# Kernel optimization log

Measured on AMD Instinct MI355X. Metric: run time of the kernel, lower is better.

The kernel has to match this reference:

```python
import jax, jax.numpy as jnp
import numpy as np

ANG = 5   # angular resolution (u = v = 5, n = 25 views)
CH = 64   # input channels
D = 2 * CH  # spa_dim + ang_dim + fre_dim = c/2 + c/2 + c = 128
NEG = -1e15


def _l2(x):
    # torch F.normalize over the contraction axis (last axis of folded layout)
    n = jnp.sqrt(jnp.sum(x * x, axis=-1, keepdims=True))
    return x / jnp.maximum(n, 1e-12)


def setup_inputs() -> dict:
    key = jax.random.key(0)
    ks = jax.random.split(key, 8)
    b, c, n, h, w = 4, CH, ANG * ANG, 32, 32
    d = D
    return {
        "x_lf": jax.random.normal(ks[0], (b, c, n, h, w), jnp.float32),
        "x_hf": jax.random.normal(ks[1], (b, c, n, h, w), jnp.float32),
        "W_in": jax.random.normal(ks[2], (c, d), jnp.float32) / np.sqrt(c).astype(np.float32),
        "W_kv": jax.random.normal(ks[3], (c, d), jnp.float32) / np.sqrt(c).astype(np.float32),
        "ln_g": jnp.ones((d,), jnp.float32),
        "ln_b": jnp.zeros((d,), jnp.float32),
        "W_m1": jax.random.normal(ks[4], (d, d), jnp.float32) / np.sqrt(d).astype(np.float32),
        "W_m2": jax.random.normal(ks[5], (d, d), jnp.float32) / np.sqrt(d).astype(np.float32),
        "W_out": jax.random.normal(ks[6], (d, c), jnp.float32) / np.sqrt(d).astype(np.float32),
    }


def _attend(fold, unfold, tq, tk, tv):
    # fold(t): (b, cc, u*v, h, w) -> (b, M, K); k/v use the same folding
    qf = _l2(fold(tq))            # q normalized over contraction axis
    kf = _l2(fold(tk))            # k normalized over contraction axis (dim=-2 of k^T)
    vf = fold(tv)
    att = jnp.einsum('bmk,bnk->bmn', qf, kf)   # (b, M, M)
    M = att.shape[-1]
    tril = jnp.tril(jnp.ones((M, M), bool))    # causal mask over folded axis
    att = jax.nn.softmax(jnp.where(tril, att, NEG), axis=-1)
    return unfold(att @ vf) + tv               # residual with token_v


def reference(x_lf, x_hf, W_in, W_kv, ln_g, ln_b, W_m1, W_m2, W_out):
    b, c, n, h, w = x_hf.shape
    u = v = ANG
    d = W_in.shape[1]

    def to_tokens(x, W):
        # 'b c (u v) h w -> (b u v) (h w) c' ; Linear ; back to 'b d (u v) h w'
        xt = x.reshape(b, c, u, v, h, w).transpose(0, 2, 3, 4, 5, 1).reshape(b * u * v, h * w, c)
        y = xt @ W
        return y.reshape(b, u, v, h, w, d).transpose(0, 5, 1, 2, 3, 4).reshape(b, d, u * v, h, w)

    q = to_tokens(x_hf, W_in)
    kv = to_tokens(x_lf, W_kv)
    cq = d // 4
    sf_q, af_q, sa_q = q[:, :cq], q[:, cq:2 * cq], q[:, 2 * cq:]
    sf_kv, af_kv, sa_kv = kv[:, :cq], kv[:, cq:2 * cq], kv[:, 2 * cq:]

    # SpatialFrequency: 'b c (u v) h w -> b (c h) (w u v)'
    def sf_fold(t):
        cc = t.shape[1]
        return t.reshape(b, cc, u, v, h, w).transpose(0, 1, 4, 5, 2, 3).reshape(b, cc * h, w * u * v)
    def sf_unfold(t):
        cc = t.shape[1] // h
        return t.reshape(b, cc, h, w, u, v).transpose(0, 1, 4, 5, 2, 3).reshape(b, cc, u * v, h, w)

    # AngularFrequency: 'b c (u v) h w -> b (c u) (h v w)'
    def af_fold(t):
        cc = t.shape[1]
        return t.reshape(b, cc, u, v, h, w).transpose(0, 1, 2, 4, 3, 5).reshape(b, cc * u, h * v * w)
    def af_unfold(t):
        cc = t.shape[1] // u
        return t.reshape(b, cc, u, h, v, w).transpose(0, 1, 2, 4, 3, 5).reshape(b, cc, u * v, h, w)

    # SpatialAngular: 'b c (u v) h w -> b (h u) (c v w)'
    def sa_fold(t):
        cc = t.shape[1]
        return t.reshape(b, cc, u, v, h, w).transpose(0, 4, 2, 1, 3, 5).reshape(b, h * u, cc * v * w)
    def sa_unfold(t):
        cc = t.shape[2] // (v * w) if t.ndim == 3 else t.shape[1]
        t = t.reshape(b, h, u, cc, v, w)
        return t.transpose(0, 3, 2, 4, 1, 5).reshape(b, cc, u * v, h, w)

    sf = _attend(sf_fold, sf_unfold, sf_q, sf_kv, sf_kv)
    af = _attend(af_fold, af_unfold, af_q, af_kv, af_kv)
    sa = _attend(sa_fold, sa_unfold, sa_q, sa_kv, sa_kv)

    cat = jnp.concatenate([sf, af, sa], axis=1)  # (b, d, n, h, w)
    ct = cat.reshape(b, d, u, v, h, w).transpose(0, 2, 3, 4, 5, 1).reshape(b * u * v, h * w, d)

    # c_mlp: LayerNorm -> Linear -> ReLU -> Linear (dropout is identity in eval)
    mu = jnp.mean(ct, axis=-1, keepdims=True)
    var = jnp.mean(jnp.square(ct - mu), axis=-1, keepdims=True)
    ln = (ct - mu) / jnp.sqrt(var + 1e-5) * ln_g + ln_b
    mlp = jax.nn.relu(ln @ W_m1) @ W_m2
    out_t = (mlp + ct) @ W_out  # residual then output projection

    out = out_t.reshape(b, u, v, h, w, -1).transpose(0, 5, 1, 2, 3, 4).reshape(b, -1, u * v, h, w)
    return out
```

## Files before the change

kernel.cpp:

```cpp
#include <hip/hip_runtime.h>

#define NSP   25600
#define HWC   1024

typedef __attribute__((ext_vector_type(8))) short bf8;
typedef __attribute__((ext_vector_type(4))) float f4;
#define MFMA(a,b,c) __builtin_amdgcn_mfma_f32_16x16x32_bf16(a, b, c, 0, 0, 0)
typedef unsigned short u16;

__device__ __forceinline__ u16 f2b(float f) {
    union { float f; unsigned u; } v; v.f = f;
    unsigned r = v.u + 0x7fffu + ((v.u >> 16) & 1u);
    return (u16)(r >> 16);
}
__device__ __forceinline__ float b2f(u16 h) {
    union { unsigned u; float f; } v; v.u = ((unsigned)h) << 16;
    return v.f;
}

__device__ __forceinline__ long row_base(int att, int b, int m) {
    if (att == 0) { int cc = m >> 5, h = m & 31;   return ((long)(b*128 + cc))*NSP + h*32; }
    else if (att == 1) { int cc = m / 5, u = m - cc*5; return ((long)(b*128 + 32 + cc))*NSP + u*5120; }
    else { int h = m / 5, u = m - h*5;            return ((long)(b*128 + 64))*NSP + u*5120 + h*32; }
}
__device__ __forceinline__ long chunk_off(int att, int kc) {
    if (att == 0) return (long)kc * 1024;
    else if (att == 1) return (long)kc * 32;
    else { int cc = kc / 5, v = kc - cc*5; return (long)cc*NSP + v*1024; }
}

__global__ __launch_bounds__(256) void k_prep(
        const float* __restrict__ Wi, const float* __restrict__ Wk,
        const float* __restrict__ W1, const float* __restrict__ W2,
        const float* __restrict__ Wo, u16* __restrict__ wbt) {
    int e = blockIdx.x * 256 + threadIdx.x;
    const float* src; int base, K, N;
    if (e < 8192)       { src = Wi; base = 0;     K = 64;  N = 128; }
    else if (e < 16384) { src = Wk; base = 8192;  K = 64;  N = 128; }
    else if (e < 32768) { src = W1; base = 16384; K = 128; N = 128; }
    else if (e < 49152) { src = W2; base = 32768; K = 128; N = 128; }
    else                { src = Wo; base = 49152; K = 128; N = 64;  }
    int local = e - base, n = local / K, k = local - n * K;
    wbt[e] = f2b(src[k * N + n]);
}

__global__ __launch_bounds__(256) void k_tokens(
        const float* __restrict__ x_hf, const float* __restrict__ x_lf,
        const u16* __restrict__ wbt,
        u16* __restrict__ qb, u16* __restrict__ kvb) {
    int s0 = blockIdx.x * 64, b = blockIdx.y, which = blockIdx.z;
    const float* x  = which ? x_lf : x_hf;
    const u16* Wb = wbt + (which ? 8192 : 0);
    u16* out = which ? kvb : qb;
    __shared__ u16 Axs[64 * 72];
    __shared__ u16 Wl [128 * 72];
    int tid = threadIdx.x;
    for (int g = tid; g < 1024; g += 256) {
        int d = g >> 3, c8 = (g & 7) * 8;
        *(bf8*)&Wl[d * 72 + c8] = *(const bf8*)(Wb + d * 64 + c8);
    }
    for (int g = tid; g < 1024; g += 256) {
        int s = g & 63, c4 = (g >> 6) * 4;
        long xb = ((long)(b * 64 + c4)) * NSP + s0 + s;
        ushort4 pk;
        pk.x = f2b(x[xb]);
        pk.y = f2b(x[xb + NSP]);
        pk.z = f2b(x[xb + 2 * NSP]);
        pk.w = f2b(x[xb + 3 * NSP]);
        *(ushort4*)&Axs[s * 72 + c4] = pk;
    }
    __syncthreads();
    int w = tid >> 6, l = tid & 63, quad = l >> 4, col = l & 15;
    f4 z = {0.f, 0.f, 0.f, 0.f};
    f4 acc[8]; for (int i = 0; i < 8; ++i) acc[i] = z;
#pragma unroll
    for (int kc = 0; kc < 2; ++kc) {
        bf8 a = *(bf8*)&Axs[(w * 16 + col) * 72 + kc * 32 + quad * 8];
#pragma unroll
        for (int nt = 0; nt < 8; ++nt) {
            bf8 bb = *(bf8*)&Wl[(nt * 16 + col) * 72 + kc * 32 + quad * 8];
            acc[nt] = MFMA(a, bb, acc[nt]);
        }
    }
#pragma unroll
    for (int nt = 0; nt < 8; ++nt) {
        int d = nt * 16 + col;
        long base = ((long)(b * 128 + d)) * NSP + s0 + w * 16 + quad * 4;
        ushort4 pk;
        pk.x = f2b(acc[nt][0]); pk.y = f2b(acc[nt][1]);
        pk.z = f2b(acc[nt][2]); pk.w = f2b(acc[nt][3]);
        *(ushort4*)(out + base) = pk;
    }
}

__global__ __launch_bounds__(256) void k_vt_norms(
        const u16* __restrict__ qb, const u16* __restrict__ kvb,
        u16* __restrict__ vt0, u16* __restrict__ vt1, u16* __restrict__ vt2,
        float* __restrict__ nq, float* __restrict__ nk) {
    int x = blockIdx.x, b = blockIdx.y;
    int tid = threadIdx.x;
    if (x < 3200) {
        int att, kc, pt, P, KC; u16* vt;
        if (x < 800)       { att = 0; kc = x >> 5; pt = (x & 31) * 32; P = 1024; KC = 25;  vt = vt0; }
        else if (x < 1600) { int x2 = x - 800;  att = 1; kc = x2 / 5; pt = (x2 - kc * 5) * 32; P = 160; KC = 160; vt = vt1; }
        else               { int x3 = x - 1600; att = 2; kc = x3 / 5; pt = (x3 - kc * 5) * 32; P = 160; KC = 320; vt = vt2; }
        long co = chunk_off(att, kc);
        __shared__ u16 T[32 * 36];
        {
            int r = tid >> 3, fq = (tid & 7) * 4;
            ushort4 e = *(const ushort4*)(kvb + row_base(att, b, pt + r) + co + fq);
            *(ushort4*)&T[r * 36 + fq] = e;
        }
        __syncthreads();
        {
            int f = tid >> 3, p4 = (tid & 7) * 4;
            ushort4 pk;
            pk.x = T[(p4    ) * 36 + f];
            pk.y = T[(p4 + 1) * 36 + f];
            pk.z = T[(p4 + 2) * 36 + f];
            pk.w = T[(p4 + 3) * 36 + f];
            *(ushort4*)(vt + ((long)b * KC + kc) * 32 * P + (long)f * P + pt + p4) = pk;
        }
    } else {
        int x2 = x - 3200;
        int which = x2 >= 336;
        int g = which ? x2 - 336 : x2;
        int att, m0, KC;
        if (g < 256)      { att = 0; m0 = g * 4;         KC = 25;  }
        else if (g < 296) { att = 1; m0 = (g - 256) * 4; KC = 160; }
        else              { att = 2; m0 = (g - 296) * 4; KC = 320; }
        const u16* src = which ? kvb : qb;
        float* dst = which ? nk : nq;
        int w = tid >> 6, lane = tid & 63;
        int m = m0 + w;
        long base = row_base(att, b, m);
        int K = KC * 32;
        float s = 0.f;
        for (int k8 = lane * 8; k8 < K; k8 += 512) {
            bf8 v = *(const bf8*)(src + base + chunk_off(att, k8 >> 5) + (k8 & 31));
#pragma unroll
            for (int j = 0; j < 8; ++j) { float f = b2f(((u16*)&v)[j]); s += f * f; }
        }
        for (int o = 32; o >= 1; o >>= 1) s += __shfl_xor(s, o);
        if (lane == 0) {
            int off = (att == 0) ? b * 1024 + m
                                 : ((att == 1) ? 4096 : 4736) + b * 160 + m;
            dst[off] = fmaxf(sqrtf(s), 1e-12f);
        }
    }
}

__global__ __launch_bounds__(256) void k_sgemm_all(
        const u16* __restrict__ qb, const u16* __restrict__ kvb,
        const float* __restrict__ nq, const float* __restrict__ nk,
        u16* __restrict__ Sb, float* __restrict__ Spart) {
    __shared__ float lds[4096];
    int x = blockIdx.x, b = blockIdx.y;
    int tid = threadIdx.x, w = tid >> 6, l = tid & 63, quad = l >> 4, col = l & 15;
    if (x < 136) {
        u16* Qs = (u16*)lds;
        u16* Ks = Qs + 64 * 40;
        int t = x, i = 0;
        while (t >= (i + 1) * (i + 2) / 2) ++i;
        int j = t - i * (i + 1) / 2;
        int mt = i * 64, nt = j * 64;
        int srow = tid >> 2, g = tid & 3;
        f4 z = {0.f, 0.f, 0.f, 0.f};
        f4 acc[4]; for (int q = 0; q < 4; ++q) acc[q] = z;
        for (int kc = 0; kc < 25; ++kc) {
            long co = (long)kc * 1024;
            {
                int m = mt + srow;
                *(bf8*)&Qs[srow * 40 + g * 8] =
                    *(const bf8*)(qb + ((long)(b*128 + (m >> 5)))*NSP + (m & 31)*32 + co + g*8);
                int n = nt + srow;
                *(bf8*)&Ks[srow * 40 + g * 8] =
                    *(const bf8*)(kvb + ((long)(b*128 + (n >> 5)))*NSP + (n & 31)*32 + co + g*8);
            }
            __syncthreads();
            bf8 a = *(bf8*)&Qs[(w * 16 + col) * 40 + quad * 8];
#pragma unroll
            for (int t2 = 0; t2 < 4; ++t2) {
                bf8 bb = *(bf8*)&Ks[(t2 * 16 + col) * 40 + quad * 8];
                acc[t2] = MFMA(a, bb, acc[t2]);
            }
            __syncthreads();
        }
#pragma unroll
        for (int t2 = 0; t2 < 4; ++t2)
#pragma unroll
            for (int r = 0; r < 4; ++r) {
                int m = mt + w * 16 + quad * 4 + r, n = nt + t2 * 16 + col;
                float v = (n <= m) ? acc[t2][r] / (nq[b*1024 + m] * nk[b*1024 + n]) : 0.f;
                Sb[((long)b * 1024 + m) * 1024 + n] = f2b(v);
            }
    } else {
        int x2 = x - 136;
        int t = x2 % 15, y = x2 / 15;
        int att, split, nsplit; float* base;
        if (y < 10) { att = 1; split = y;      nsplit = 10; base = Spart; }
        else        { att = 2; split = y - 10; nsplit = 20; base = Spart + 614400; }
        int i = 0;
        while (t >= (i + 1) * (i + 2) / 2) ++i;
        int j = t - i * (i + 1) / 2;
        int mt = i * 32, nt = j * 32;
        long rm0 = row_base(att, b, mt + col),      rm1 = row_base(att, b, mt + 16 + col);
        long rn0 = row_base(att, b, nt + col),      rn1 = row_base(att, b, nt + 16 + col);
        int ko = quad * 8;
        f4 z = {0.f, 0.f, 0.f, 0.f};
        f4 a00 = z, a01 = z, a10 = z, a11 = z;
#pragma unroll
        for (int s = 0; s < 4; ++s) {
            int kc = split * 16 + w * 4 + s;
            long co = chunk_off(att, kc);
            bf8 qa0 = *(const bf8*)(qb + rm0 + co + ko);
            bf8 qa1 = *(const bf8*)(qb + rm1 + co + ko);
            bf8 kb0 = *(const bf8*)(kvb + rn0 + co + ko);
            bf8 kb1 = *(const bf8*)(kvb + rn1 + co + ko);
            a00 = MFMA(qa0, kb0, a00); a01 = MFMA(qa0, kb1, a01);
            a10 = MFMA(qa1, kb0, a10); a11 = MFMA(qa1, kb1, a11);
        }
        float* my = lds + w * 1024;
#pragma unroll
        for (int r = 0; r < 4; ++r) {
            my[(quad * 4 + r) * 32 + col]            = a00[r];
            my[(quad * 4 + r) * 32 + 16 + col]       = a01[r];
            my[(16 + quad * 4 + r) * 32 + col]       = a10[r];
            my[(16 + quad * 4 + r) * 32 + 16 + col]  = a11[r];
        }
        __syncthreads();
        float* dst = base + ((long)((b * 15 + t) * nsplit + split)) * 1024;
        for (int e = tid; e < 1024; e += 256)
            dst[e] = lds[e] + lds[1024 + e] + lds[2048 + e] + lds[3072 + e];
    }
}

__global__ __launch_bounds__(256) void k_softmax_all(
        const u16* __restrict__ Sb, u16* __restrict__ Pb,
        const float* __restrict__ Spart, const float* __restrict__ nq,
        const float* __restrict__ nk, u16* __restrict__ Pb12) {
    int xb = blockIdx.x, b = blockIdx.y, tid = threadIdx.x;
    if (xb < 256) {
        int w = tid >> 6, lane = tid & 63;
        int m = xb * 4 + w;
        const u16* row = Sb + ((long)b * 1024 + m) * 1024;
        u16* pr = Pb + ((long)b * 1024 + m) * 1024;
        int e0 = lane * 16;
        bf8 x0 = *(const bf8*)(row + e0);
        bf8 x1 = *(const bf8*)(row + e0 + 8);
        float v[16];
#pragma unroll
        for (int j = 0; j < 8; ++j) { v[j] = b2f(((u16*)&x0)[j]); v[8 + j] = b2f(((u16*)&x1)[j]); }
        float mx = -1e30f;
#pragma unroll
        for (int j = 0; j < 16; ++j) if (e0 + j <= m) mx = fmaxf(mx, v[j]);
#pragma unroll
        for (int o = 32; o >= 1; o >>= 1) mx = fmaxf(mx, __shfl_xor(mx, o));
        float s = 0.f;
#pragma unroll
        for (int j = 0; j < 16; ++j) {
            float e = (e0 + j <= m) ? __expf(v[j] - mx) : 0.f;
            v[j] = e; s += e;
        }
#pragma unroll
        for (int o = 32; o >= 1; o >>= 1) s += __shfl_xor(s, o);
        float inv = 1.f / s;
        bf8 o0, o1;
#pragma unroll
        for (int j = 0; j < 8; ++j) {
            ((u16*)&o0)[j] = f2b(v[j] * inv);
            ((u16*)&o1)[j] = f2b(v[8 + j] * inv);
        }
        *(bf8*)(pr + e0) = o0;
        *(bf8*)(pr + e0 + 8) = o1;
    } else {
        int x = xb - 256;
        int att = (x < 160) ? 1 : 2;
        int m = (att == 1) ? x : x - 160;
        int nsplit = (att == 1) ? 10 : 20;
        const float* base = (att == 1) ? Spart : Spart + 614400;
        int noff = (att == 1) ? 4096 : 4736;
        u16* P = Pb12 + ((att == 1) ? 0 : 102400);
        int i = m >> 5, ro = (m & 31) * 32;
        int n = tid;
        bool act = (n <= m) && (n < 160);
        float myv = 0.f;
        if (act) {
            int t = i * (i + 1) / 2 + (n >> 5);
            const float* src = base + ((long)((b * 15 + t) * nsplit)) * 1024 + ro + (n & 31);
            float s = 0.f;
            for (int sp = 0; sp < nsplit; ++sp) s += src[(long)sp * 1024];
            myv = s / (nq[noff + b * 160 + m] * nk[noff + b * 160 + n]);
        }
        __shared__ float red[256];
        red[tid] = act ? myv : -1e30f; __syncthreads();
        for (int w = 128; w >= 1; w >>= 1) {
            if (tid < w) red[tid] = fmaxf(red[tid], red[tid + w]);
            __syncthreads();
        }
        float mx = red[0]; __syncthreads();
        float e = act ? __expf(myv - mx) : 0.f;
        red[tid] = e; __syncthreads();
        for (int w = 128; w >= 1; w >>= 1) {
            if (tid < w) red[tid] += red[tid + w];
            __syncthreads();
        }
        float inv = 1.f / red[0];
        if (n < 160) P[((long)b * 160 + m) * 160 + n] = f2b(e * inv);
    }
}

__global__ __launch_bounds__(256) void k_ogemm_all(
        const u16* __restrict__ Pb, const u16* __restrict__ vt0,
        const u16* __restrict__ Pb12, const u16* __restrict__ vt1,
        const u16* __restrict__ vt2, const u16* __restrict__ kvb,
        u16* __restrict__ catb) {
    __shared__ __align__(16) u16 lds[64 * 72 + 32 * 72];
    int x = blockIdx.x, b = blockIdx.y;
    int tid = threadIdx.x, w = tid >> 6, l = tid & 63, quad = l >> 4, col = l & 15;
    if (x < 400) {
        int mtt = x & 15, kc = x >> 4;
        int mt = mtt * 64;
        long co = (long)kc * 1024;
        const u16* vtc = vt0 + ((long)b * 25 + kc) * 32 * 1024;
        u16* Ps = lds;
        u16* Vs = lds + 64 * 72;
        f4 z = {0.f, 0.f, 0.f, 0.f};
        f4 acc[2]; acc[0] = z; acc[1] = z;
        for (int s = 0; s <= mtt; ++s) {
            int p0 = s * 64;
#pragma unroll
            for (int i = 0; i < 2; ++i) {
                int idx = i * 256 + tid;
                int row = idx >> 3, c8 = (idx & 7) * 8;
                *(bf8*)&Ps[row * 72 + c8] =
                    *(const bf8*)(Pb + ((long)(b * 1024 + mt + row)) * 1024 + p0 + c8);
            }
            {
                int f = tid >> 3, p8 = (tid & 7) * 8;
                *(bf8*)&Vs[f * 72 + p8] =
                    *(const bf8*)(vtc + (long)f * 1024 + p0 + p8);
            }
            __syncthreads();
            bf8 a0 = *(bf8*)&Ps[(w * 16 + col) * 72 + quad * 8];
            bf8 a1 = *(bf8*)&Ps[(w * 16 + col) * 72 + 32 + quad * 8];
#pragma unroll
            for (int t2 = 0; t2 < 2; ++t2) {
                bf8 b0 = *(bf8*)&Vs[(t2 * 16 + col) * 72 + quad * 8];
                bf8 b1 = *(bf8*)&Vs[(t2 * 16 + col) * 72 + 32 + quad * 8];
                acc[t2] = MFMA(a0, b0, acc[t2]);
                acc[t2] = MFMA(a1, b1, acc[t2]);
            }
            __syncthreads();
        }
#pragma unroll
        for (int t2 = 0; t2 < 2; ++t2)
#pragma unroll
            for (int r = 0; r < 4; ++r) {
                int m = mt + w * 16 + quad * 4 + r, f = t2 * 16 + col;
                long adr = ((long)(b * 128 + (m >> 5))) * NSP + (m & 31) * 32 + co + f;
                catb[adr] = f2b(acc[t2][r] + b2f(kvb[adr]));
            }
    } else {
        int x2 = x - 400;
        int att = (x2 < 320) ? 1 : 2;
        int ft  = (att == 1) ? x2 : x2 - 320;
        int KC  = (att == 1) ? 160 : 320;
        const u16* vt = (att == 1) ? vt1 : vt2;
        const u16* Prow = Pb12 + ((att == 1) ? 0 : 102400) + (long)b * 160 * 160;
        u16* Vs = lds;
        for (int g = tid; g < 320; g += 256) {
            int fl = g / 20, p8 = (g % 20) * 8;
            int fglob = ft * 16 + fl;
            int kc = fglob >> 5, fr = fglob & 31;
            *(bf8*)&Vs[fl * 168 + p8] =
                *(const bf8*)(vt + (((long)b * KC + kc) * 32 + fr) * 160 + p8);
        }
        __syncthreads();
        int fglob = ft * 16 + col;
        int kcf = fglob >> 5, fi = fglob & 31;
        long cbase = chunk_off(att, kcf) + fi;
        f4 z = {0.f, 0.f, 0.f, 0.f};
        for (int j = 0; j < 3; ++j) {
            int mi = w + 4 * j;
            if (mi >= 10) break;
            int nkk = (mi >> 1) + 1;
            f4 acc = z;
#pragma unroll 5
            for (int kk = 0; kk < nkk; ++kk) {
                bf8 a  = *(const bf8*)(Prow + (mi * 16 + col) * 160 + kk * 32 + quad * 8);
                bf8 bb = *(bf8*)&Vs[col * 168 + kk * 32 + quad * 8];
                acc = MFMA(a, bb, acc);
            }
#pragma unroll
            for (int r = 0; r < 4; ++r) {
                int m = mi * 16 + quad * 4 + r;
                long adr = row_base(att, b, m) + cbase;
                catb[adr] = f2b(acc[r] + b2f(kvb[adr]));
            }
        }
    }
}

__global__ __launch_bounds__(256) void k_transpose_ln(
        const u16* __restrict__ catb, u16* __restrict__ ctb,
        float* __restrict__ mu, float* __restrict__ rstd) {
    int hwt = blockIdx.x * 16, bn = blockIdx.y;
    int b = bn / 25, uv = bn - b * 25;
    __shared__ u16 T[16 * 136];
    int tid = threadIdx.x;
    const u16* src = catb + (long)b * 128 * NSP + (long)uv * HWC + hwt;
    {
        int d = tid >> 1, hw8 = (tid & 1) * 8;
        bf8 v = *(const bf8*)(src + (long)d * NSP + hw8);
#pragma unroll
        for (int j = 0; j < 8; ++j) T[(hw8 + j) * 136 + d] = ((u16*)&v)[j];
    }
    __syncthreads();
    {
        int w = tid >> 6, l = tid & 63;
        int tk = w * 4 + (l >> 4), dg = (l & 15) * 8;
        bf8 vv = *(bf8*)&T[tk * 136 + dg];
        float s = 0.f, s2 = 0.f;
#pragma unroll
        for (int j = 0; j < 8; ++j) {
            float f = b2f(((u16*)&vv)[j]); s += f; s2 += f * f;
        }
        for (int o = 8; o >= 1; o >>= 1) { s += __shfl_xor(s, o); s2 += __shfl_xor(s2, o); }
        if ((l & 15) == 0) {
            int t = bn * 1024 + hwt + tk;
            float m = s * (1.f / 128.f);
            float var = s2 * (1.f / 128.f) - m * m;
            mu[t] = m; rstd[t] = rsqrtf(var + 1e-5f);
        }
    }
    {
        int hw = tid >> 4, d8 = (tid & 15) * 8;
        *(bf8*)(ctb + ((long)(bn * 1024 + hwt + hw)) * 128 + d8) = *(bf8*)&T[hw * 136 + d8];
    }
}

__global__ __launch_bounds__(256) void k_mlp1(
        const u16* __restrict__ ctb, const float* __restrict__ mu,
        const float* __restrict__ rstd, const float* __restrict__ g,
        const float* __restrict__ be, const u16* __restrict__ wbt,
        u16* __restrict__ h1b) {
    int tt = blockIdx.x * 64, tid = threadIdx.x;
    const u16* W1b = wbt + 16384;
    __shared__ u16 As[64 * 136], Wt[128 * 136];
    __shared__ float gl[128], bl[128];
    if (tid < 128) { gl[tid] = g[tid]; bl[tid] = be[tid]; }
    for (int q = tid; q < 2048; q += 256) {
        int n = q >> 4, k8 = (q & 15) * 8;
        *(bf8*)&Wt[n * 136 + k8] = *(const bf8*)(W1b + n * 128 + k8);
    }
    __syncthreads();
    for (int q = tid; q < 1024; q += 256) {
        int row = q >> 4, k8 = (q & 15) * 8, t = tt + row;
        bf8 cv = *(const bf8*)(ctb + (long)t * 128 + k8);
        float m = mu[t], rs = rstd[t];
        bf8 av;
#pragma unroll
        for (int j = 0; j < 8; ++j)
            ((u16*)&av)[j] = f2b((b2f(((u16*)&cv)[j]) - m) * rs * gl[k8 + j] + bl[k8 + j]);
        *(bf8*)&As[row * 136 + k8] = av;
    }
    __syncthreads();
    int w = tid >> 6, l = tid & 63, quad = l >> 4, col = l & 15;
    f4 z = {0.f, 0.f, 0.f, 0.f};
    f4 acc[8]; for (int i = 0; i < 8; ++i) acc[i] = z;
#pragma unroll
    for (int kc = 0; kc < 4; ++kc) {
        bf8 a = *(bf8*)&As[(w * 16 + col) * 136 + kc * 32 + quad * 8];
#pragma unroll
        for (int nt = 0; nt < 8; ++nt) {
            bf8 bb = *(bf8*)&Wt[(nt * 16 + col) * 136 + kc * 32 + quad * 8];
            acc[nt] = MFMA(a, bb, acc[nt]);
        }
    }
#pragma unroll
    for (int nt = 0; nt < 8; ++nt)
#pragma unroll
        for (int r = 0; r < 4; ++r) {
            int t = tt + w * 16 + quad * 4 + r, n = nt * 16 + col;
            h1b[(long)t * 128 + n] = f2b(fmaxf(acc[nt][r], 0.f));
        }
}

__global__ __launch_bounds__(256) void k_mlp2(
        const u16* __restrict__ h1b, const u16* __restrict__ ctb,
        const u16* __restrict__ wbt, u16* __restrict__ m2b) {
    int tt = blockIdx.x * 64, tid = threadIdx.x;
    const u16* W2b = wbt + 32768;
    __shared__ u16 As[64 * 136], Wt[128 * 136];
    for (int q = tid; q < 2048; q += 256) {
        int n = q >> 4, k8 = (q & 15) * 8;
        *(bf8*)&Wt[n * 136 + k8] = *(const bf8*)(W2b + n * 128 + k8);
    }
    for (int q = tid; q < 1024; q += 256) {
        int row = q >> 4, k8 = (q & 15) * 8;
        *(bf8*)&As[row * 136 + k8] = *(const bf8*)(h1b + (long)(tt + row) * 128 + k8);
    }
    __syncthreads();
    int w = tid >> 6, l = tid & 63, quad = l >> 4, col = l & 15;
    f4 z = {0.f, 0.f, 0.f, 0.f};
    f4 acc[8]; for (int i = 0; i < 8; ++i) acc[i] = z;
#pragma unroll
    for (int kc = 0; kc < 4; ++kc) {
        bf8 a = *(bf8*)&As[(w * 16 + col) * 136 + kc * 32 + quad * 8];
#pragma unroll
        for (int nt = 0; nt < 8; ++nt) {
            bf8 bb = *(bf8*)&Wt[(nt * 16 + col) * 136 + kc * 32 + quad * 8];
            acc[nt] = MFMA(a, bb, acc[nt]);
        }
    }
#pragma unroll
    for (int nt = 0; nt < 8; ++nt)
#pragma unroll
        for (int r = 0; r < 4; ++r) {
            int t = tt + w * 16 + quad * 4 + r, n = nt * 16 + col;
            m2b[(long)t * 128 + n] = f2b(acc[nt][r] + b2f(ctb[(long)t * 128 + n]));
        }
}

__global__ __launch_bounds__(256) void k_out(
        const u16* __restrict__ m2b, const u16* __restrict__ wbt,
        float* __restrict__ out) {
    int tt = blockIdx.x * 64, tid = threadIdx.x;
    const u16* Wob = wbt + 49152;
    __shared__ u16 As[64 * 136], Wt[64 * 136];
    for (int q = tid; q < 1024; q += 256) {
        int o = q >> 4, k8 = (q & 15) * 8;
        *(bf8*)&Wt[o * 136 + k8] = *(const bf8*)(Wob + o * 128 + k8);
    }
    for (int q = tid; q < 1024; q += 256) {
        int row = q >> 4, k8 = (q & 15) * 8;
        *(bf8*)&As[row * 136 + k8] = *(const bf8*)(m2b + (long)(tt + row) * 128 + k8);
    }
    __syncthreads();
    int w = tid >> 6, l = tid & 63, quad = l >> 4, col = l & 15;
    f4 z = {0.f, 0.f, 0.f, 0.f};
    f4 acc[4]; for (int i = 0; i < 4; ++i) acc[i] = z;
#pragma unroll
    for (int kc = 0; kc < 4; ++kc) {
        bf8 a = *(bf8*)&As[(w * 16 + col) * 136 + kc * 32 + quad * 8];
#pragma unroll
        for (int nt = 0; nt < 4; ++nt) {
            bf8 bb = *(bf8*)&Wt[(nt * 16 + col) * 136 + kc * 32 + quad * 8];
            acc[nt] = MFMA(a, bb, acc[nt]);
        }
    }
    int t0 = tt + w * 16 + quad * 4;
    int bn = t0 >> 10, hw = t0 & 1023;
    int b = bn / 25, uv = bn - b * 25;
#pragma unroll
    for (int nt = 0; nt < 4; ++nt) {
        int o = nt * 16 + col;
        float4 pk = {acc[nt][0], acc[nt][1], acc[nt][2], acc[nt][3]};
        *(float4*)(out + ((long)((b * 64 + o) * 25 + uv)) * 1024 + hw) = pk;
    }
}

extern "C" void kernel_launch(void* const* d_in, const int* in_sizes, int n_in,
                              void* d_out, int out_size, void* d_ws, size_t ws_size,
                              hipStream_t stream) {
    const float* x_lf = (const float*)d_in[0];
    const float* x_hf = (const float*)d_in[1];
    const float* W_in = (const float*)d_in[2];
    const float* W_kv = (const float*)d_in[3];
    const float* ln_g = (const float*)d_in[4];
    const float* ln_b = (const float*)d_in[5];
    const float* W_m1 = (const float*)d_in[6];
    const float* W_m2 = (const float*)d_in[7];
    const float* W_ot = (const float*)d_in[8];
    float* out = (float*)d_out;

    float* ws = (float*)d_ws;
    u16*   qb    = (u16*)ws;
    u16*   h1b   = qb;
    u16*   kvb   = (u16*)(ws + 6553600);
    u16*   m2b   = kvb;
    u16*   catb  = (u16*)(ws + 13107200);
    u16*   ctb   = (u16*)(ws + 19660800);
    u16*   Sb    = (u16*)(ws + 26214400);
    u16*   Pb    = (u16*)(ws + 28311552);
    u16*   Pb12  = (u16*)(ws + 30408704);
    float* Spart = ws + 30511104;
    float* nq    = ws + 32354304;
    float* nk    = ws + 32359680;
    float* mu    = ws + 32365056;
    float* rstd  = ws + 32467456;
    u16*   vt0   = (u16*)(ws + 32569856);
    u16*   vt1   = (u16*)(ws + 34208256);
    u16*   vt2   = (u16*)(ws + 35846656);
    u16*   wbt   = (u16*)(ws + 39123456);

    k_prep<<<dim3(224), 256, 0, stream>>>(W_in, W_kv, W_m1, W_m2, W_ot, wbt);

    k_tokens<<<dim3(400, 4, 2), 256, 0, stream>>>(x_hf, x_lf, wbt, qb, kvb);

    k_vt_norms<<<dim3(3872, 4), 256, 0, stream>>>(qb, kvb, vt0, vt1, vt2, nq, nk);

    k_sgemm_all<<<dim3(586, 4), 256, 0, stream>>>(qb, kvb, nq, nk, Sb, Spart);

    k_softmax_all<<<dim3(576, 4), 256, 0, stream>>>(Sb, Pb, Spart, nq, nk, Pb12);

    k_ogemm_all<<<dim3(1360, 4), 256, 0, stream>>>(Pb, vt0, Pb12, vt1, vt2, kvb, catb);

    k_transpose_ln<<<dim3(64, 100), 256, 0, stream>>>(catb, ctb, mu, rstd);

    k_mlp1<<<dim3(1600), 256, 0, stream>>>(ctb, mu, rstd, ln_g, ln_b, wbt, h1b);
    k_mlp2<<<dim3(1600), 256, 0, stream>>>(h1b, ctb, wbt, m2b);
    k_out <<<dim3(1600), 256, 0, stream>>>(m2b, wbt, out);
}
```

Before: 310.3 us.

## Load MFMA operands directly from global and widen vt0 transpose tiles

The spatial-frequency score GEMM and output GEMM now load bf16 MFMA fragments straight from global memory into registers, dropping the LDS staging and the two barriers per k-step. The vt0 transpose in the norms kernel now handles 128-row tiles per block, which cuts the grid size. This removes LDS round-trips and synchronisation, but each wave now issues separate strided global loads, and operands that blocks used to share through LDS are read redundantly, relying on cache hits.

```diff
diff --git a/kernel.cpp b/kernel.cpp
--- a/kernel.cpp
+++ b/kernel.cpp
@@ -99,13 +99,34 @@
         float* __restrict__ nq, float* __restrict__ nk) {
     int x = blockIdx.x, b = blockIdx.y;
     int tid = threadIdx.x;
-    if (x < 3200) {
-        int att, kc, pt, P, KC; u16* vt;
-        if (x < 800)       { att = 0; kc = x >> 5; pt = (x & 31) * 32; P = 1024; KC = 25;  vt = vt0; }
-        else if (x < 1600) { int x2 = x - 800;  att = 1; kc = x2 / 5; pt = (x2 - kc * 5) * 32; P = 160; KC = 160; vt = vt1; }
-        else               { int x3 = x - 1600; att = 2; kc = x3 / 5; pt = (x3 - kc * 5) * 32; P = 160; KC = 320; vt = vt2; }
+    __shared__ u16 T[128 * 36];
+    if (x < 200) {
+        int kc = x >> 3, pt = (x & 7) * 128;
+        long co = (long)kc * 1024;
+#pragma unroll
+        for (int i = 0; i < 4; ++i) {
+            int idx = i * 256 + tid;
+            int r = idx >> 3, fq = (idx & 7) * 4;
+            ushort4 e = *(const ushort4*)(kvb + row_base(0, b, pt + r) + co + fq);
+            *(ushort4*)&T[r * 36 + fq] = e;
+        }
+        __syncthreads();
+#pragma unroll
+        for (int i = 0; i < 4; ++i) {
+            int idx = i * 256 + tid;
+            int f = idx >> 5, p4 = (idx & 31) * 4;
+            ushort4 pk;
+            pk.x = T[(p4    ) * 36 + f];
+            pk.y = T[(p4 + 1) * 36 + f];
+            pk.z = T[(p4 + 2) * 36 + f];
+            pk.w = T[(p4 + 3) * 36 + f];
+            *(ushort4*)(vt0 + (((long)b * 25 + kc) * 32 + f) * 1024 + pt + p4) = pk;
+        }
+    } else if (x < 2600) {
+        int att, kc, pt, KC; u16* vt;
+        if (x < 1000) { int x2 = x - 200;  att = 1; kc = x2 / 5; pt = (x2 - kc * 5) * 32; KC = 160; vt = vt1; }
+        else          { int x3 = x - 1000; att = 2; kc = x3 / 5; pt = (x3 - kc * 5) * 32; KC = 320; vt = vt2; }
         long co = chunk_off(att, kc);
-        __shared__ u16 T[32 * 36];
         {
             int r = tid >> 3, fq = (tid & 7) * 4;
             ushort4 e = *(const ushort4*)(kvb + row_base(att, b, pt + r) + co + fq);
@@ -119,10 +140,10 @@
             pk.y = T[(p4 + 1) * 36 + f];
             pk.z = T[(p4 + 2) * 36 + f];
             pk.w = T[(p4 + 3) * 36 + f];
-            *(ushort4*)(vt + ((long)b * KC + kc) * 32 * P + (long)f * P + pt + p4) = pk;
+            *(ushort4*)(vt + (((long)b * KC + kc) * 32 + f) * 160 + pt + p4) = pk;
         }
     } else {
-        int x2 = x - 3200;
+        int x2 = x - 2600;
         int which = x2 >= 336;
         int g = which ? x2 - 336 : x2;
         int att, m0, KC;
@@ -158,41 +179,39 @@
     int x = blockIdx.x, b = blockIdx.y;
     int tid = threadIdx.x, w = tid >> 6, l = tid & 63, quad = l >> 4, col = l & 15;
     if (x < 136) {
-        u16* Qs = (u16*)lds;
-        u16* Ks = Qs + 64 * 40;
         int t = x, i = 0;
         while (t >= (i + 1) * (i + 2) / 2) ++i;
         int j = t - i * (i + 1) / 2;
         int mt = i * 64, nt = j * 64;
-        int srow = tid >> 2, g = tid & 3;
+        int m = mt + w * 16 + col;
+        long qoff = ((long)(b * 128 + (m >> 5))) * NSP + (m & 31) * 32 + quad * 8;
+        int n0 = nt + col, n1 = nt + 16 + col, n2 = nt + 32 + col, n3 = nt + 48 + col;
+        long koff0 = ((long)(b * 128 + (n0 >> 5))) * NSP + (n0 & 31) * 32 + quad * 8;
+        long koff1 = ((long)(b * 128 + (n1 >> 5))) * NSP + (n1 & 31) * 32 + quad * 8;
+        long koff2 = ((long)(b * 128 + (n2 >> 5))) * NSP + (n2 & 31) * 32 + quad * 8;
+        long koff3 = ((long)(b * 128 + (n3 >> 5))) * NSP + (n3 & 31) * 32 + quad * 8;
         f4 z = {0.f, 0.f, 0.f, 0.f};
         f4 acc[4]; for (int q = 0; q < 4; ++q) acc[q] = z;
+#pragma unroll 2
         for (int kc = 0; kc < 25; ++kc) {
             long co = (long)kc * 1024;
-            {
-                int m = mt + srow;
-                *(bf8*)&Qs[srow * 40 + g * 8] =
-                    *(const bf8*)(qb + ((long)(b*128 + (m >> 5)))*NSP + (m & 31)*32 + co + g*8);
-                int n = nt + srow;
-                *(bf8*)&Ks[srow * 40 + g * 8] =
-                    *(const bf8*)(kvb + ((long)(b*128 + (n >> 5)))*NSP + (n & 31)*32 + co + g*8);
-            }
-            __syncthreads();
-            bf8 a = *(bf8*)&Qs[(w * 16 + col) * 40 + quad * 8];
-#pragma unroll
-            for (int t2 = 0; t2 < 4; ++t2) {
-                bf8 bb = *(bf8*)&Ks[(t2 * 16 + col) * 40 + quad * 8];
-                acc[t2] = MFMA(a, bb, acc[t2]);
-            }
-            __syncthreads();
+            bf8 a  = *(const bf8*)(qb + qoff + co);
+            bf8 b0 = *(const bf8*)(kvb + koff0 + co);
+            bf8 b1 = *(const bf8*)(kvb + koff1 + co);
+            bf8 b2 = *(const bf8*)(kvb + koff2 + co);
+            bf8 b3 = *(const bf8*)(kvb + koff3 + co);
+            acc[0] = MFMA(a, b0, acc[0]);
+            acc[1] = MFMA(a, b1, acc[1]);
+            acc[2] = MFMA(a, b2, acc[2]);
+            acc[3] = MFMA(a, b3, acc[3]);
         }
 #pragma unroll
         for (int t2 = 0; t2 < 4; ++t2)
 #pragma unroll
             for (int r = 0; r < 4; ++r) {
-                int m = mt + w * 16 + quad * 4 + r, n = nt + t2 * 16 + col;
-                float v = (n <= m) ? acc[t2][r] / (nq[b*1024 + m] * nk[b*1024 + n]) : 0.f;
-                Sb[((long)b * 1024 + m) * 1024 + n] = f2b(v);
+                int mm = mt + w * 16 + quad * 4 + r, nn = nt + t2 * 16 + col;
+                float v = (nn <= mm) ? acc[t2][r] / (nq[b*1024 + mm] * nk[b*1024 + nn]) : 0.f;
+                Sb[((long)b * 1024 + mm) * 1024 + nn] = f2b(v);
             }
     } else {
         int x2 = x - 136;
@@ -315,7 +334,7 @@
         const u16* __restrict__ Pb12, const u16* __restrict__ vt1,
         const u16* __restrict__ vt2, const u16* __restrict__ kvb,
         u16* __restrict__ catb) {
-    __shared__ __align__(16) u16 lds[64 * 72 + 32 * 72];
+    __shared__ __align__(16) u16 lds[16 * 168];
     int x = blockIdx.x, b = blockIdx.y;
     int tid = threadIdx.x, w = tid >> 6, l = tid & 63, quad = l >> 4, col = l & 15;
     if (x < 400) {
@@ -323,42 +342,29 @@
         int mt = mtt * 64;
         long co = (long)kc * 1024;
         const u16* vtc = vt0 + ((long)b * 25 + kc) * 32 * 1024;
-        u16* Ps = lds;
-        u16* Vs = lds + 64 * 72;
+        int m = mt + w * 16 + col;
+        const u16* pr = Pb + ((long)(b * 1024 + m)) * 1024 + quad * 8;
+        const u16* v0 = vtc + (long)col * 1024 + quad * 8;
+        const u16* v1 = vtc + (long)(16 + col) * 1024 + quad * 8;
         f4 z = {0.f, 0.f, 0.f, 0.f};
         f4 acc[2]; acc[0] = z; acc[1] = z;
         for (int s = 0; s <= mtt; ++s) {
             int p0 = s * 64;
-#pragma unroll
-            for (int i = 0; i < 2; ++i) {
-                int idx = i * 256 + tid;
-                int row = idx >> 3, c8 = (idx & 7) * 8;
-                *(bf8*)&Ps[row * 72 + c8] =
-                    *(const bf8*)(Pb + ((long)(b * 1024 + mt + row)) * 1024 + p0 + c8);
-            }
-            {
-                int f = tid >> 3, p8 = (tid & 7) * 8;
-                *(bf8*)&Vs[f * 72 + p8] =
-                    *(const bf8*)(vtc + (long)f * 1024 + p0 + p8);
-            }
-            __syncthreads();
-            bf8 a0 = *(bf8*)&Ps[(w * 16 + col) * 72 + quad * 8];
-            bf8 a1 = *(bf8*)&Ps[(w * 16 + col) * 72 + 32 + quad * 8];
-#pragma unroll
-            for (int t2 = 0; t2 < 2; ++t2) {
-                bf8 b0 = *(bf8*)&Vs[(t2 * 16 + col) * 72 + quad * 8];
-                bf8 b1 = *(bf8*)&Vs[(t2 * 16 + col) * 72 + 32 + quad * 8];
-                acc[t2] = MFMA(a0, b0, acc[t2]);
-                acc[t2] = MFMA(a1, b1, acc[t2]);
-            }
-            __syncthreads();
+            bf8 a0  = *(const bf8*)(pr + p0);
+            bf8 a1  = *(const bf8*)(pr + p0 + 32);
+            bf8 b00 = *(const bf8*)(v0 + p0);
+            bf8 b01 = *(const bf8*)(v0 + p0 + 32);
+            bf8 b10 = *(const bf8*)(v1 + p0);
+            bf8 b11 = *(const bf8*)(v1 + p0 + 32);
+            acc[0] = MFMA(a0, b00, acc[0]); acc[0] = MFMA(a1, b01, acc[0]);
+            acc[1] = MFMA(a0, b10, acc[1]); acc[1] = MFMA(a1, b11, acc[1]);
         }
 #pragma unroll
         for (int t2 = 0; t2 < 2; ++t2)
 #pragma unroll
             for (int r = 0; r < 4; ++r) {
-                int m = mt + w * 16 + quad * 4 + r, f = t2 * 16 + col;
-                long adr = ((long)(b * 128 + (m >> 5))) * NSP + (m & 31) * 32 + co + f;
+                int mm = mt + w * 16 + quad * 4 + r, f = t2 * 16 + col;
+                long adr = ((long)(b * 128 + (mm >> 5))) * NSP + (mm & 31) * 32 + co + f;
                 catb[adr] = f2b(acc[t2][r] + b2f(kvb[adr]));
             }
     } else {
@@ -599,7 +605,7 @@
 
     k_tokens<<<dim3(400, 4, 2), 256, 0, stream>>>(x_hf, x_lf, wbt, qb, kvb);
 
-    k_vt_norms<<<dim3(3872, 4), 256, 0, stream>>>(qb, kvb, vt0, vt1, vt2, nq, nk);
+    k_vt_norms<<<dim3(3272, 4), 256, 0, stream>>>(qb, kvb, vt0, vt1, vt2, nq, nk);
 
     k_sgemm_all<<<dim3(586, 4), 256, 0, stream>>>(qb, kvb, nq, nk, Sb, Spart);
 
```

Measured after the change: 372.3 us. 20.0% more time.

## Fuse LayerNorm and MLP into one kernel with precomputed W_m2·W_out

Applied to the files above, without the earlier changes.

Replaces the transpose/LayerNorm, two MLP GEMMs and output projection kernels with one fused kernel that keeps each 64-token tile in shared memory. It uses the algebraic identity (mlp+ct)@Wo = ct@Wo + relu(..)@(W2@Wo), with the product W2·Wo precomputed by a small prep kernel. This removes several intermediate bf16 round trips through global memory and two launches. It also widens the att0 V-transpose blocks to 128 rows. Rounding changes because W2·Wo is formed in fp32 and then stored as bf16.

```diff
diff --git a/kernel.cpp b/kernel.cpp
--- a/kernel.cpp
+++ b/kernel.cpp
@@ -42,6 +42,16 @@
     else                { src = Wo; base = 49152; K = 128; N = 64;  }
     int local = e - base, n = local / K, k = local - n * K;
     wbt[e] = f2b(src[k * N + n]);
+}
+
+__global__ __launch_bounds__(256) void k_prep2(
+        const float* __restrict__ W2, const float* __restrict__ Wo,
+        u16* __restrict__ w2o) {
+    int e = blockIdx.x * 256 + threadIdx.x;
+    int o = e >> 7, k = e & 127;
+    float s = 0.f;
+    for (int n = 0; n < 128; ++n) s += W2[k * 128 + n] * Wo[n * 64 + o];
+    w2o[e] = f2b(s);
 }
 
 __global__ __launch_bounds__(256) void k_tokens(
@@ -99,13 +109,34 @@
         float* __restrict__ nq, float* __restrict__ nk) {
     int x = blockIdx.x, b = blockIdx.y;
     int tid = threadIdx.x;
-    if (x < 3200) {
-        int att, kc, pt, P, KC; u16* vt;
-        if (x < 800)       { att = 0; kc = x >> 5; pt = (x & 31) * 32; P = 1024; KC = 25;  vt = vt0; }
-        else if (x < 1600) { int x2 = x - 800;  att = 1; kc = x2 / 5; pt = (x2 - kc * 5) * 32; P = 160; KC = 160; vt = vt1; }
-        else               { int x3 = x - 1600; att = 2; kc = x3 / 5; pt = (x3 - kc * 5) * 32; P = 160; KC = 320; vt = vt2; }
+    __shared__ u16 T[128 * 36];
+    if (x < 200) {
+        int kc = x >> 3, pt = (x & 7) * 128;
+        long co = (long)kc * 1024;
+#pragma unroll
+        for (int i = 0; i < 4; ++i) {
+            int idx = i * 256 + tid;
+            int r = idx >> 3, fq = (idx & 7) * 4;
+            ushort4 e = *(const ushort4*)(kvb + row_base(0, b, pt + r) + co + fq);
+            *(ushort4*)&T[r * 36 + fq] = e;
+        }
+        __syncthreads();
+#pragma unroll
+        for (int i = 0; i < 4; ++i) {
+            int idx = i * 256 + tid;
+            int f = idx >> 5, p4 = (idx & 31) * 4;
+            ushort4 pk;
+            pk.x = T[(p4    ) * 36 + f];
+            pk.y = T[(p4 + 1) * 36 + f];
+            pk.z = T[(p4 + 2) * 36 + f];
+            pk.w = T[(p4 + 3) * 36 + f];
+            *(ushort4*)(vt0 + (((long)b * 25 + kc) * 32 + f) * 1024 + pt + p4) = pk;
+        }
+    } else if (x < 2600) {
+        int att, kc, pt, KC; u16* vt;
+        if (x < 1000) { int x2 = x - 200;  att = 1; kc = x2 / 5; pt = (x2 - kc * 5) * 32; KC = 160; vt = vt1; }
+        else          { int x3 = x - 1000; att = 2; kc = x3 / 5; pt = (x3 - kc * 5) * 32; KC = 320; vt = vt2; }
         long co = chunk_off(att, kc);
-        __shared__ u16 T[32 * 36];
         {
             int r = tid >> 3, fq = (tid & 7) * 4;
             ushort4 e = *(const ushort4*)(kvb + row_base(att, b, pt + r) + co + fq);
@@ -119,10 +150,10 @@
             pk.y = T[(p4 + 1) * 36 + f];
             pk.z = T[(p4 + 2) * 36 + f];
             pk.w = T[(p4 + 3) * 36 + f];
-            *(ushort4*)(vt + ((long)b * KC + kc) * 32 * P + (long)f * P + pt + p4) = pk;
+            *(ushort4*)(vt + (((long)b * KC + kc) * 32 + f) * 160 + pt + p4) = pk;
         }
     } else {
-        int x2 = x - 3200;
+        int x2 = x - 2600;
         int which = x2 >= 336;
         int g = which ? x2 - 336 : x2;
         int att, m0, KC;
@@ -402,161 +433,120 @@
     }
 }
 
-__global__ __launch_bounds__(256) void k_transpose_ln(
-        const u16* __restrict__ catb, u16* __restrict__ ctb,
-        float* __restrict__ mu, float* __restrict__ rstd) {
-    int hwt = blockIdx.x * 16, bn = blockIdx.y;
+__global__ __launch_bounds__(256) void k_mlp_fused(
+        const u16* __restrict__ catb, const float* __restrict__ g,
+        const float* __restrict__ be, const u16* __restrict__ wbt,
+        const u16* __restrict__ w2o, float* __restrict__ out) {
+    int x = blockIdx.x, tid = threadIdx.x;
+    int tt = x * 64;
+    int bn = tt >> 10, hwt = tt & 1023;
     int b = bn / 25, uv = bn - b * 25;
-    __shared__ u16 T[16 * 136];
-    int tid = threadIdx.x;
+    __shared__ u16 CT[64 * 136];
+    __shared__ u16 Wt[128 * 136];
+    __shared__ float gl[128], bl[128], mu_s[64], rs_s[64];
+    int w = tid >> 6, l = tid & 63, quad = l >> 4, col = l & 15;
     const u16* src = catb + (long)b * 128 * NSP + (long)uv * HWC + hwt;
+#pragma unroll
+    for (int i = 0; i < 4; ++i) {
+        int gi = i * 256 + tid;
+        int d = gi >> 3, hw8 = (gi & 7) * 8;
+        bf8 v = *(const bf8*)(src + (long)d * NSP + hw8);
+#pragma unroll
+        for (int j = 0; j < 8; ++j) CT[(hw8 + j) * 136 + d] = ((u16*)&v)[j];
+    }
     {
-        int d = tid >> 1, hw8 = (tid & 1) * 8;
-        bf8 v = *(const bf8*)(src + (long)d * NSP + hw8);
-#pragma unroll
-        for (int j = 0; j < 8; ++j) T[(hw8 + j) * 136 + d] = ((u16*)&v)[j];
-    }
+        const u16* Wob = wbt + 49152;
+        for (int q = tid; q < 1024; q += 256) {
+            int o = q >> 4, k8 = (q & 15) * 8;
+            *(bf8*)&Wt[o * 136 + k8] = *(const bf8*)(Wob + o * 128 + k8);
+        }
+    }
+    if (tid < 128) { gl[tid] = g[tid]; bl[tid] = be[tid]; }
     __syncthreads();
+    f4 z = {0.f, 0.f, 0.f, 0.f};
+    f4 acc_o[4]; for (int i = 0; i < 4; ++i) acc_o[i] = z;
+#pragma unroll
+    for (int kc = 0; kc < 4; ++kc) {
+        bf8 a = *(bf8*)&CT[(w * 16 + col) * 136 + kc * 32 + quad * 8];
+#pragma unroll
+        for (int nt = 0; nt < 4; ++nt) {
+            bf8 bb = *(bf8*)&Wt[(nt * 16 + col) * 136 + kc * 32 + quad * 8];
+            acc_o[nt] = MFMA(a, bb, acc_o[nt]);
+        }
+    }
     {
-        int w = tid >> 6, l = tid & 63;
-        int tk = w * 4 + (l >> 4), dg = (l & 15) * 8;
-        bf8 vv = *(bf8*)&T[tk * 136 + dg];
+        int tk = w * 16 + (l >> 2), dg = (l & 3) * 32;
         float s = 0.f, s2 = 0.f;
 #pragma unroll
-        for (int j = 0; j < 8; ++j) {
-            float f = b2f(((u16*)&vv)[j]); s += f; s2 += f * f;
-        }
-        for (int o = 8; o >= 1; o >>= 1) { s += __shfl_xor(s, o); s2 += __shfl_xor(s2, o); }
-        if ((l & 15) == 0) {
-            int t = bn * 1024 + hwt + tk;
+        for (int q = 0; q < 4; ++q) {
+            bf8 vv = *(bf8*)&CT[tk * 136 + dg + q * 8];
+#pragma unroll
+            for (int j = 0; j < 8; ++j) { float f = b2f(((u16*)&vv)[j]); s += f; s2 += f * f; }
+        }
+        s += __shfl_xor(s, 1); s2 += __shfl_xor(s2, 1);
+        s += __shfl_xor(s, 2); s2 += __shfl_xor(s2, 2);
+        if ((l & 3) == 0) {
             float m = s * (1.f / 128.f);
             float var = s2 * (1.f / 128.f) - m * m;
-            mu[t] = m; rstd[t] = rsqrtf(var + 1e-5f);
-        }
-    }
-    {
-        int hw = tid >> 4, d8 = (tid & 15) * 8;
-        *(bf8*)(ctb + ((long)(bn * 1024 + hwt + hw)) * 128 + d8) = *(bf8*)&T[hw * 136 + d8];
-    }
-}
-
-__global__ __launch_bounds__(256) void k_mlp1(
-        const u16* __restrict__ ctb, const float* __restrict__ mu,
-        const float* __restrict__ rstd, const float* __restrict__ g,
-        const float* __restrict__ be, const u16* __restrict__ wbt,
-        u16* __restrict__ h1b) {
-    int tt = blockIdx.x * 64, tid = threadIdx.x;
-    const u16* W1b = wbt + 16384;
-    __shared__ u16 As[64 * 136], Wt[128 * 136];
-    __shared__ float gl[128], bl[128];
-    if (tid < 128) { gl[tid] = g[tid]; bl[tid] = be[tid]; }
-    for (int q = tid; q < 2048; q += 256) {
-        int n = q >> 4, k8 = (q & 15) * 8;
-        *(bf8*)&Wt[n * 136 + k8] = *(const bf8*)(W1b + n * 128 + k8);
+            mu_s[tk] = m; rs_s[tk] = rsqrtf(var + 1e-5f);
+        }
     }
     __syncthreads();
     for (int q = tid; q < 1024; q += 256) {
-        int row = q >> 4, k8 = (q & 15) * 8, t = tt + row;
-        bf8 cv = *(const bf8*)(ctb + (long)t * 128 + k8);
-        float m = mu[t], rs = rstd[t];
+        int row = q >> 4, k8 = (q & 15) * 8;
+        bf8 cv = *(bf8*)&CT[row * 136 + k8];
+        float m = mu_s[row], rs = rs_s[row];
         bf8 av;
 #pragma unroll
         for (int j = 0; j < 8; ++j)
             ((u16*)&av)[j] = f2b((b2f(((u16*)&cv)[j]) - m) * rs * gl[k8 + j] + bl[k8 + j]);
-        *(bf8*)&As[row * 136 + k8] = av;
+        *(bf8*)&CT[row * 136 + k8] = av;
+    }
+    {
+        const u16* W1b = wbt + 16384;
+        for (int q = tid; q < 2048; q += 256) {
+            int n = q >> 4, k8 = (q & 15) * 8;
+            *(bf8*)&Wt[n * 136 + k8] = *(const bf8*)(W1b + n * 128 + k8);
+        }
     }
     __syncthreads();
-    int w = tid >> 6, l = tid & 63, quad = l >> 4, col = l & 15;
-    f4 z = {0.f, 0.f, 0.f, 0.f};
-    f4 acc[8]; for (int i = 0; i < 8; ++i) acc[i] = z;
+    f4 acc_h[8]; for (int i = 0; i < 8; ++i) acc_h[i] = z;
 #pragma unroll
     for (int kc = 0; kc < 4; ++kc) {
-        bf8 a = *(bf8*)&As[(w * 16 + col) * 136 + kc * 32 + quad * 8];
+        bf8 a = *(bf8*)&CT[(w * 16 + col) * 136 + kc * 32 + quad * 8];
 #pragma unroll
         for (int nt = 0; nt < 8; ++nt) {
             bf8 bb = *(bf8*)&Wt[(nt * 16 + col) * 136 + kc * 32 + quad * 8];
-            acc[nt] = MFMA(a, bb, acc[nt]);
-        }
-    }
+            acc_h[nt] = MFMA(a, bb, acc_h[nt]);
+        }
+    }
+    __syncthreads();
 #pragma unroll
     for (int nt = 0; nt < 8; ++nt)
 #pragma unroll
         for (int r = 0; r < 4; ++r) {
-            int t = tt + w * 16 + quad * 4 + r, n = nt * 16 + col;
-            h1b[(long)t * 128 + n] = f2b(fmaxf(acc[nt][r], 0.f));
-        }
-}
-
-__global__ __launch_bounds__(256) void k_mlp2(
-        const u16* __restrict__ h1b, const u16* __restrict__ ctb,
-        const u16* __restrict__ wbt, u16* __restrict__ m2b) {
-    int tt = blockIdx.x * 64, tid = threadIdx.x;
-    const u16* W2b = wbt + 32768;
-    __shared__ u16 As[64 * 136], Wt[128 * 136];
-    for (int q = tid; q < 2048; q += 256) {
-        int n = q >> 4, k8 = (q & 15) * 8;
-        *(bf8*)&Wt[n * 136 + k8] = *(const bf8*)(W2b + n * 128 + k8);
-    }
-    for (int q = tid; q < 1024; q += 256) {
-        int row = q >> 4, k8 = (q & 15) * 8;
-        *(bf8*)&As[row * 136 + k8] = *(const bf8*)(h1b + (long)(tt + row) * 128 + k8);
-    }
-    __syncthreads();
-    int w = tid >> 6, l = tid & 63, quad = l >> 4, col = l & 15;
-    f4 z = {0.f, 0.f, 0.f, 0.f};
-    f4 acc[8]; for (int i = 0; i < 8; ++i) acc[i] = z;
-#pragma unroll
-    for (int kc = 0; kc < 4; ++kc) {
-        bf8 a = *(bf8*)&As[(w * 16 + col) * 136 + kc * 32 + quad * 8];
-#pragma unroll
-        for (int nt = 0; nt < 8; ++nt) {
-            bf8 bb = *(bf8*)&Wt[(nt * 16 + col) * 136 + kc * 32 + quad * 8];
-            acc[nt] = MFMA(a, bb, acc[nt]);
-        }
-    }
-#pragma unroll
-    for (int nt = 0; nt < 8; ++nt)
-#pragma unroll
-        for (int r = 0; r < 4; ++r) {
-            int t = tt + w * 16 + quad * 4 + r, n = nt * 16 + col;
-            m2b[(long)t * 128 + n] = f2b(acc[nt][r] + b2f(ctb[(long)t * 128 + n]));
-        }
-}
-
-__global__ __launch_bounds__(256) void k_out(
-        const u16* __restrict__ m2b, const u16* __restrict__ wbt,
-        float* __restrict__ out) {
-    int tt = blockIdx.x * 64, tid = threadIdx.x;
-    const u16* Wob = wbt + 49152;
-    __shared__ u16 As[64 * 136], Wt[64 * 136];
+            int row = w * 16 + quad * 4 + r, n = nt * 16 + col;
+            CT[row * 136 + n] = f2b(fmaxf(acc_h[nt][r], 0.f));
+        }
     for (int q = tid; q < 1024; q += 256) {
         int o = q >> 4, k8 = (q & 15) * 8;
-        *(bf8*)&Wt[o * 136 + k8] = *(const bf8*)(Wob + o * 128 + k8);
-    }
-    for (int q = tid; q < 1024; q += 256) {
-        int row = q >> 4, k8 = (q & 15) * 8;
-        *(bf8*)&As[row * 136 + k8] = *(const bf8*)(m2b + (long)(tt + row) * 128 + k8);
+        *(bf8*)&Wt[o * 136 + k8] = *(const bf8*)(w2o + o * 128 + k8);
     }
     __syncthreads();
-    int w = tid >> 6, l = tid & 63, quad = l >> 4, col = l & 15;
-    f4 z = {0.f, 0.f, 0.f, 0.f};
-    f4 acc[4]; for (int i = 0; i < 4; ++i) acc[i] = z;
 #pragma unroll
     for (int kc = 0; kc < 4; ++kc) {
-        bf8 a = *(bf8*)&As[(w * 16 + col) * 136 + kc * 32 + quad * 8];
+        bf8 a = *(bf8*)&CT[(w * 16 + col) * 136 + kc * 32 + quad * 8];
 #pragma unroll
         for (int nt = 0; nt < 4; ++nt) {
             bf8 bb = *(bf8*)&Wt[(nt * 16 + col) * 136 + kc * 32 + quad * 8];
-            acc[nt] = MFMA(a, bb, acc[nt]);
-        }
-    }
-    int t0 = tt + w * 16 + quad * 4;
-    int bn = t0 >> 10, hw = t0 & 1023;
-    int b = bn / 25, uv = bn - b * 25;
+            acc_o[nt] = MFMA(a, bb, acc_o[nt]);
+        }
+    }
+    int hw = hwt + w * 16 + quad * 4;
 #pragma unroll
     for (int nt = 0; nt < 4; ++nt) {
         int o = nt * 16 + col;
-        float4 pk = {acc[nt][0], acc[nt][1], acc[nt][2], acc[nt][3]};
+        float4 pk = {acc_o[nt][0], acc_o[nt][1], acc_o[nt][2], acc_o[nt][3]};
         *(float4*)(out + ((long)((b * 64 + o) * 25 + uv)) * 1024 + hw) = pk;
     }
 }
@@ -577,29 +567,26 @@
 
     float* ws = (float*)d_ws;
     u16*   qb    = (u16*)ws;
-    u16*   h1b   = qb;
     u16*   kvb   = (u16*)(ws + 6553600);
-    u16*   m2b   = kvb;
     u16*   catb  = (u16*)(ws + 13107200);
-    u16*   ctb   = (u16*)(ws + 19660800);
     u16*   Sb    = (u16*)(ws + 26214400);
     u16*   Pb    = (u16*)(ws + 28311552);
     u16*   Pb12  = (u16*)(ws + 30408704);
     float* Spart = ws + 30511104;
     float* nq    = ws + 32354304;
     float* nk    = ws + 32359680;
-    float* mu    = ws + 32365056;
-    float* rstd  = ws + 32467456;
+    u16*   w2ob  = (u16*)(ws + 32365056);
     u16*   vt0   = (u16*)(ws + 32569856);
     u16*   vt1   = (u16*)(ws + 34208256);
     u16*   vt2   = (u16*)(ws + 35846656);
     u16*   wbt   = (u16*)(ws + 39123456);
 
     k_prep<<<dim3(224), 256, 0, stream>>>(W_in, W_kv, W_m1, W_m2, W_ot, wbt);
+    k_prep2<<<dim3(32), 256, 0, stream>>>(W_m2, W_ot, w2ob);
 
     k_tokens<<<dim3(400, 4, 2), 256, 0, stream>>>(x_hf, x_lf, wbt, qb, kvb);
 
-    k_vt_norms<<<dim3(3872, 4), 256, 0, stream>>>(qb, kvb, vt0, vt1, vt2, nq, nk);
+    k_vt_norms<<<dim3(3272, 4), 256, 0, stream>>>(qb, kvb, vt0, vt1, vt2, nq, nk);
 
     k_sgemm_all<<<dim3(586, 4), 256, 0, stream>>>(qb, kvb, nq, nk, Sb, Spart);
 
@@ -607,9 +594,5 @@
 
     k_ogemm_all<<<dim3(1360, 4), 256, 0, stream>>>(Pb, vt0, Pb12, vt1, vt2, kvb, catb);
 
-    k_transpose_ln<<<dim3(64, 100), 256, 0, stream>>>(catb, ctb, mu, rstd);
-
-    k_mlp1<<<dim3(1600), 256, 0, stream>>>(ctb, mu, rstd, ln_g, ln_b, wbt, h1b);
-    k_mlp2<<<dim3(1600), 256, 0, stream>>>(h1b, ctb, wbt, m2b);
-    k_out <<<dim3(1600), 256, 0, stream>>>(m2b, wbt, out);
-}
+    k_mlp_fused<<<dim3(1600), 256, 0, stream>>>(catb, ln_g, ln_b, wbt, w2ob, out);
+}
```

Measured after the change: 275.5 us. 11.2% less time.
